# Performance work log

Measured on AMD Instinct MI355X. Metric: run time of the kernel, lower is better.

The kernel has to match this reference:

```python
import jax, jax.numpy as jnp
import numpy as np

LN_EPS = 1e-5

def setup_inputs() -> dict:
    key = jax.random.key(0)
    k1, k2, k3, k4 = jax.random.split(key, 4)
    B, S, D, P = 8, 4096, 1024, 512
    return {
        "hidden_states": jax.random.normal(k1, (B, S, D), dtype=jnp.float32),
        "ln_weight": jnp.ones((D,), dtype=jnp.float32),
        "ln_bias": jnp.zeros((D,), dtype=jnp.float32),
        "W": jax.random.normal(k2, (D, P), dtype=jnp.float32) * 0.02,  # torch Linear weight [out, in]
        "b": jnp.zeros((D,), dtype=jnp.float32),
        "s3_index": jax.random.randint(k3, (P,), 0, D, dtype=jnp.int32),
        "s5_index": jax.random.randint(k4, (D,), 0, D, dtype=jnp.int32),
    }

def reference(hidden_states, ln_weight, ln_bias, W, b, s3_index, s5_index):
    # LayerNorm over last dim
    mu = jnp.mean(hidden_states, axis=-1, keepdims=True)
    var = jnp.mean(jnp.square(hidden_states - mu), axis=-1, keepdims=True)
    normed = (hidden_states - mu) * jax.lax.rsqrt(var + LN_EPS) * ln_weight + ln_bias
    # gather pruned channels, small GEMM 512 -> 1024
    gathered = normed[..., s3_index]                      # [B, S, 512]
    h = jnp.einsum('bsp,dp->bsd', gathered, W) + b        # [B, S, 1024]
    # scatter-add into residual (duplicate indices accumulate, like index_add)
    out = hidden_states.at[..., s5_index].add(h)
    return out
```

## Files before the change

kernel.cpp:

```cpp
#include <hip/hip_runtime.h>
#include <hip/hip_bf16.h>
#include <stdint.h>

#define LN_EPS 1e-5f

typedef __attribute__((ext_vector_type(4))) float f32x4;
typedef __attribute__((ext_vector_type(8))) short bf16x8;

#define D_ 1024
#define P_ 512
#define N_ 32768

__device__ __forceinline__ void gload_lds16(const void* gsrc, void* ldst) {
  __builtin_amdgcn_global_load_lds(
      (const __attribute__((address_space(1))) void*)gsrc,
      (__attribute__((address_space(3))) void*)ldst,
      16, 0, 0);
}

__global__ void k_scatter(const float* __restrict__ W, const float* __restrict__ bias,
                          const int* __restrict__ s5,
                          float* __restrict__ w2f, float* __restrict__ b2) {
  int d = blockIdx.x;
  int c = s5[d];
  const float* wrow = W + (size_t)d * P_;
  float* dst = w2f + (size_t)c * P_;
  for (int p = threadIdx.x; p < P_; p += 256)
    atomicAdd(&dst[p], wrow[p]);
  if (threadIdx.x == 0) atomicAdd(&b2[c], bias[d]);
}

__global__ void k_conv(const float* __restrict__ w2f, __hip_bfloat16* __restrict__ w2b) {
  int i = blockIdx.x * 256 + threadIdx.x;
  if (i < D_ * P_) w2b[i] = __float2bfloat16(w2f[i]);
}

__global__ __launch_bounds__(256) void k_ln_gather(
    const float* __restrict__ x, const float* __restrict__ lnw,
    const float* __restrict__ lnb, const int* __restrict__ s3,
    __hip_bfloat16* __restrict__ g) {
  __shared__ float row[D_];
  __shared__ float psum[4], psum2[4];
  const int n = blockIdx.x;
  const int t = threadIdx.x;
  const float* xr = x + (size_t)n * D_;
  float4 v = ((const float4*)xr)[t];
  ((float4*)row)[t] = v;
  float s  = v.x + v.y + v.z + v.w;
  float s2 = v.x*v.x + v.y*v.y + v.z*v.z + v.w*v.w;
  #pragma unroll
  for (int off = 32; off > 0; off >>= 1) {
    s  += __shfl_down(s, off);
    s2 += __shfl_down(s2, off);
  }
  const int lane = t & 63, wid = t >> 6;
  if (lane == 0) { psum[wid] = s; psum2[wid] = s2; }
  __syncthreads();
  const float tot  = psum[0] + psum[1] + psum[2] + psum[3];
  const float tot2 = psum2[0] + psum2[1] + psum2[2] + psum2[3];
  const float mu  = tot * (1.f / D_);
  const float var = tot2 * (1.f / D_) - mu * mu;
  const float inv = rsqrtf(var + LN_EPS);
  __hip_bfloat16* gr = g + (size_t)n * P_;
  const int i0 = s3[2*t], i1 = s3[2*t+1];
  const float v0 = (row[i0] - mu) * inv * lnw[i0] + lnb[i0];
  const float v1 = (row[i1] - mu) * inv * lnw[i1] + lnb[i1];
  union { __hip_bfloat16 h; unsigned short u; } c0, c1;
  c0.h = __float2bfloat16(v0);
  c1.h = __float2bfloat16(v1);
  unsigned int packed = (unsigned int)c0.u | ((unsigned int)c1.u << 16);
  ((unsigned int*)gr)[t] = packed;
}

#define BM 128
#define BN 128
#define BK 64

__global__ __launch_bounds__(512, 4) void k_gemm(
    const __hip_bfloat16* __restrict__ g,
    const __hip_bfloat16* __restrict__ w2b,
    const float* __restrict__ b2,
    const float* __restrict__ hid,
    float* __restrict__ out) {
  __shared__ __align__(16) char smem[65536];
  char* At[2] = { smem,         smem + 16384 };
  char* Bt[2] = { smem + 32768, smem + 49152 };
  float* ctile = (float*)smem;

  const int bid = blockIdx.x;
  const int x = bid & 7;
  const int kq = bid >> 3;
  const int bm = (x * 32 + (kq >> 3)) * BM;
  const int bn = (kq & 7) * BN;

  const int t = threadIdx.x;
  const int lane = t & 63;
  const int wid = t >> 6;
  const int wr = wid >> 2, wc = wid & 3;

  f32x4 acc[4][2] = {};

  #define STAGE(ks, buf)                                                      \
    {                                                                         \
      const int k0 = (ks) * BK;                                               \
      _Pragma("unroll")                                                       \
      for (int i = 0; i < 2; ++i) {                                           \
        int ch = t + i * 512;                                     \
        int r  = ch >> 3;                      \
        int cc = ch & 7;                                                      \
        int col = ((cc ^ (r & 7)) << 3);       \
        gload_lds16(g   + (size_t)(bm + r) * P_ + k0 + col, At[buf] + ch * 16); \
        gload_lds16(w2b + (size_t)(bn + r) * P_ + k0 + col, Bt[buf] + ch * 16); \
      }                                                                       \
    }

  STAGE(0, 0);
  for (int ks = 0; ks < 8; ++ks) {
    const int buf = ks & 1;
    __syncthreads();
    if (ks < 7) STAGE(ks + 1, buf ^ 1);

    bf16x8 af[2][4], bfr[2][2];
    #pragma unroll
    for (int kk = 0; kk < 2; ++kk) {
      const int colb = kk * 64 + ((lane >> 4) << 4);
      #pragma unroll
      for (int mi = 0; mi < 4; ++mi) {
        const int r = wr * 64 + mi * 16 + (lane & 15);
        af[kk][mi] = *(const bf16x8*)(At[buf] + ((r * 128 + colb) ^ ((r & 7) << 4)));
      }
      #pragma unroll
      for (int ni = 0; ni < 2; ++ni) {
        const int r = wc * 32 + ni * 16 + (lane & 15);
        bfr[kk][ni] = *(const bf16x8*)(Bt[buf] + ((r * 128 + colb) ^ ((r & 7) << 4)));
      }
    }
    #pragma unroll
    for (int kk = 0; kk < 2; ++kk)
      #pragma unroll
      for (int mi = 0; mi < 4; ++mi)
        #pragma unroll
        for (int ni = 0; ni < 2; ++ni)
          acc[mi][ni] = __builtin_amdgcn_mfma_f32_16x16x32_bf16(
              af[kk][mi], bfr[kk][ni], acc[kk ? mi : mi][ni], 0, 0, 0);
  }

  __syncthreads();
  #pragma unroll
  for (int ni = 0; ni < 2; ++ni) {
    #pragma unroll
    for (int mi = 0; mi < 4; ++mi) {
      #pragma unroll
      for (int r4 = 0; r4 < 4; ++r4) {
        const int row = wr * 64 + mi * 16 + ((lane >> 4) << 2) + r4;
        const int col = wc * 32 + ni * 16 + (lane & 15);
        ctile[row * 128 + (col ^ (((row >> 2) & 1) << 4))] = acc[mi][ni][r4];
      }
    }
  }
  __syncthreads();
  #pragma unroll
  for (int i = 0; i < 8; ++i) {
    const int idx = i * 512 + t;
    const int row = idx >> 5;
    const int j0  = (idx & 31) << 2;
    const int swz = ((row >> 2) & 1) << 4;
    const f32x4 a = *(const f32x4*)&ctile[row * 128 + (j0 ^ swz)];
    const f32x4 bias = *(const f32x4*)(b2 + bn + j0);
    const size_t gidx = (size_t)(bm + row) * D_ + bn + j0;
    const f32x4 h = __builtin_nontemporal_load((const f32x4*)(hid + gidx));
    f32x4 o;
    o.x = h.x + a.x + bias.x;
    o.y = h.y + a.y + bias.y;
    o.z = h.z + a.z + bias.z;
    o.w = h.w + a.w + bias.w;
    __builtin_nontemporal_store(o, (f32x4*)(out + gidx));
  }
}

extern "C" void kernel_launch(void* const* d_in, const int* in_sizes, int n_in,
                              void* d_out, int out_size, void* d_ws, size_t ws_size,
                              hipStream_t stream) {
  const float* hid  = (const float*)d_in[0];
  const float* lnw  = (const float*)d_in[1];
  const float* lnb  = (const float*)d_in[2];
  const float* W    = (const float*)d_in[3];
  const float* bias = (const float*)d_in[4];
  const int*   s3   = (const int*)d_in[5];
  const int*   s5   = (const int*)d_in[6];
  float* out = (float*)d_out;

  char* ws = (char*)d_ws;
  float*          w2f = (float*)ws;
  float*          b2  = (float*)(ws + 2097152);
  __hip_bfloat16* w2b = (__hip_bfloat16*)(ws + 2101248);
  __hip_bfloat16* g   = (__hip_bfloat16*)(ws + 3149824);

  hipMemsetAsync(ws, 0, 2101248, stream);
  k_scatter<<<dim3(1024), dim3(256), 0, stream>>>(W, bias, s5, w2f, b2);
  k_conv   <<<dim3(2048), dim3(256), 0, stream>>>(w2f, w2b);
  k_ln_gather<<<dim3(N_), dim3(256), 0, stream>>>(hid, lnw, lnb, s3, g);
  k_gemm   <<<dim3(2048), dim3(512), 0, stream>>>(g, w2b, b2, hid, out);
}
```

Baseline: 122.0 us.

## Replace atomic weight scatter with gather kernel and batch LayerNorm rows per wave

Removes the memset, the atomic scatter kernel and the fp32-to-bf16 conversion kernel. They are replaced by one kernel in which each output channel scans s5 in shared memory and sums the matching W rows directly into bf16. The LayerNorm kernel now processes four rows per wave with no block-level sync, loads the gathered ln weight and bias once per thread, and writes 16-byte bf16 vectors. The goal is fewer launches, no atomics, and less per-row overhead in LN, at the cost of a 1024-iteration serial scan per channel in the weight kernel.

```diff
diff --git a/kernel.cpp b/kernel.cpp
--- a/kernel.cpp
+++ b/kernel.cpp
@@ -18,58 +18,83 @@
       16, 0, 0);
 }
 
-__global__ void k_scatter(const float* __restrict__ W, const float* __restrict__ bias,
-                          const int* __restrict__ s5,
-                          float* __restrict__ w2f, float* __restrict__ b2) {
-  int d = blockIdx.x;
-  int c = s5[d];
-  const float* wrow = W + (size_t)d * P_;
-  float* dst = w2f + (size_t)c * P_;
-  for (int p = threadIdx.x; p < P_; p += 256)
-    atomicAdd(&dst[p], wrow[p]);
-  if (threadIdx.x == 0) atomicAdd(&b2[c], bias[d]);
-}
-
-__global__ void k_conv(const float* __restrict__ w2f, __hip_bfloat16* __restrict__ w2b) {
-  int i = blockIdx.x * 256 + threadIdx.x;
-  if (i < D_ * P_) w2b[i] = __float2bfloat16(w2f[i]);
-}
-
-__global__ __launch_bounds__(256) void k_ln_gather(
+__device__ __forceinline__ short f2bf(float x) {
+  union { __hip_bfloat16 h; short s; } u; u.h = __float2bfloat16(x); return u.s;
+}
+
+__global__ __launch_bounds__(256) void k_w2(
+    const float* __restrict__ W, const float* __restrict__ bias,
+    const int* __restrict__ s5,
+    __hip_bfloat16* __restrict__ w2b, float* __restrict__ b2) {
+  __shared__ int s5l[1024];
+  const int c = blockIdx.x;
+  const int t = threadIdx.x;
+  #pragma unroll
+  for (int i = 0; i < 4; ++i) s5l[t + i * 256] = s5[t + i * 256];
+  __syncthreads();
+  float a0 = 0.f, a1 = 0.f, bb = 0.f;
+  for (int d = 0; d < 1024; ++d) {
+    if (s5l[d] == c) {
+      const float2 wv = ((const float2*)(W + (size_t)d * P_))[t];
+      a0 += wv.x; a1 += wv.y; bb += bias[d];
+    }
+  }
+  const unsigned lo = (unsigned short)f2bf(a0);
+  const unsigned hi = (unsigned short)f2bf(a1);
+  ((unsigned int*)w2b)[c * 256 + t] = lo | (hi << 16);
+  if (t == 0) b2[c] = bb;
+}
+
+__global__ __launch_bounds__(256) void k_ln(
     const float* __restrict__ x, const float* __restrict__ lnw,
     const float* __restrict__ lnb, const int* __restrict__ s3,
     __hip_bfloat16* __restrict__ g) {
-  __shared__ float row[D_];
-  __shared__ float psum[4], psum2[4];
-  const int n = blockIdx.x;
+  __shared__ __align__(16) float rowbuf[4][D_];
   const int t = threadIdx.x;
-  const float* xr = x + (size_t)n * D_;
-  float4 v = ((const float4*)xr)[t];
-  ((float4*)row)[t] = v;
-  float s  = v.x + v.y + v.z + v.w;
-  float s2 = v.x*v.x + v.y*v.y + v.z*v.z + v.w*v.w;
-  #pragma unroll
-  for (int off = 32; off > 0; off >>= 1) {
-    s  += __shfl_down(s, off);
-    s2 += __shfl_down(s2, off);
-  }
   const int lane = t & 63, wid = t >> 6;
-  if (lane == 0) { psum[wid] = s; psum2[wid] = s2; }
-  __syncthreads();
-  const float tot  = psum[0] + psum[1] + psum[2] + psum[3];
-  const float tot2 = psum2[0] + psum2[1] + psum2[2] + psum2[3];
-  const float mu  = tot * (1.f / D_);
-  const float var = tot2 * (1.f / D_) - mu * mu;
-  const float inv = rsqrtf(var + LN_EPS);
-  __hip_bfloat16* gr = g + (size_t)n * P_;
-  const int i0 = s3[2*t], i1 = s3[2*t+1];
-  const float v0 = (row[i0] - mu) * inv * lnw[i0] + lnb[i0];
-  const float v1 = (row[i1] - mu) * inv * lnw[i1] + lnb[i1];
-  union { __hip_bfloat16 h; unsigned short u; } c0, c1;
-  c0.h = __float2bfloat16(v0);
-  c1.h = __float2bfloat16(v1);
-  unsigned int packed = (unsigned int)c0.u | ((unsigned int)c1.u << 16);
-  ((unsigned int*)gr)[t] = packed;
+  float* rb = rowbuf[wid];
+
+  const int4 i0 = ((const int4*)s3)[lane * 2];
+  const int4 i1 = ((const int4*)s3)[lane * 2 + 1];
+  float wv[8], av[8];
+  wv[0]=lnw[i0.x]; wv[1]=lnw[i0.y]; wv[2]=lnw[i0.z]; wv[3]=lnw[i0.w];
+  wv[4]=lnw[i1.x]; wv[5]=lnw[i1.y]; wv[6]=lnw[i1.z]; wv[7]=lnw[i1.w];
+  av[0]=lnb[i0.x]; av[1]=lnb[i0.y]; av[2]=lnb[i0.z]; av[3]=lnb[i0.w];
+  av[4]=lnb[i1.x]; av[5]=lnb[i1.y]; av[6]=lnb[i1.z]; av[7]=lnb[i1.w];
+
+  const int nbase = blockIdx.x * 16 + wid * 4;
+  for (int rr = 0; rr < 4; ++rr) {
+    const int n = nbase + rr;
+    const float* xr = x + (size_t)n * D_;
+    f32x4 v[4];
+    #pragma unroll
+    for (int j = 0; j < 4; ++j) v[j] = ((const f32x4*)xr)[j * 64 + lane];
+    float s = 0.f, s2 = 0.f;
+    #pragma unroll
+    for (int j = 0; j < 4; ++j) {
+      s  += v[j].x + v[j].y + v[j].z + v[j].w;
+      s2 += v[j].x*v[j].x + v[j].y*v[j].y + v[j].z*v[j].z + v[j].w*v[j].w;
+    }
+    #pragma unroll
+    for (int j = 0; j < 4; ++j) ((f32x4*)rb)[j * 64 + lane] = v[j];
+    #pragma unroll
+    for (int off = 32; off > 0; off >>= 1) {
+      s  += __shfl_xor(s, off);
+      s2 += __shfl_xor(s2, off);
+    }
+    const float mu  = s * (1.f / D_);
+    const float inv = rsqrtf(s2 * (1.f / D_) - mu * mu + LN_EPS);
+    bf16x8 gv;
+    gv[0] = f2bf((rb[i0.x] - mu) * inv * wv[0] + av[0]);
+    gv[1] = f2bf((rb[i0.y] - mu) * inv * wv[1] + av[1]);
+    gv[2] = f2bf((rb[i0.z] - mu) * inv * wv[2] + av[2]);
+    gv[3] = f2bf((rb[i0.w] - mu) * inv * wv[3] + av[3]);
+    gv[4] = f2bf((rb[i1.x] - mu) * inv * wv[4] + av[4]);
+    gv[5] = f2bf((rb[i1.y] - mu) * inv * wv[5] + av[5]);
+    gv[6] = f2bf((rb[i1.z] - mu) * inv * wv[6] + av[6]);
+    gv[7] = f2bf((rb[i1.w] - mu) * inv * wv[7] + av[7]);
+    *(bf16x8*)(g + (size_t)n * P_ + lane * 8) = gv;
+  }
 }
 
 #define BM 128
@@ -142,7 +167,7 @@
         #pragma unroll
         for (int ni = 0; ni < 2; ++ni)
           acc[mi][ni] = __builtin_amdgcn_mfma_f32_16x16x32_bf16(
-              af[kk][mi], bfr[kk][ni], acc[kk ? mi : mi][ni], 0, 0, 0);
+              af[kk][mi], bfr[kk][ni], acc[mi][ni], 0, 0, 0);
   }
 
   __syncthreads();
@@ -191,14 +216,11 @@
   float* out = (float*)d_out;
 
   char* ws = (char*)d_ws;
-  float*          w2f = (float*)ws;
-  float*          b2  = (float*)(ws + 2097152);
-  __hip_bfloat16* w2b = (__hip_bfloat16*)(ws + 2101248);
-  __hip_bfloat16* g   = (__hip_bfloat16*)(ws + 3149824);
-
-  hipMemsetAsync(ws, 0, 2101248, stream);
-  k_scatter<<<dim3(1024), dim3(256), 0, stream>>>(W, bias, s5, w2f, b2);
-  k_conv   <<<dim3(2048), dim3(256), 0, stream>>>(w2f, w2b);
-  k_ln_gather<<<dim3(N_), dim3(256), 0, stream>>>(hid, lnw, lnb, s3, g);
-  k_gemm   <<<dim3(2048), dim3(512), 0, stream>>>(g, w2b, b2, hid, out);
-}
+  __hip_bfloat16* w2b = (__hip_bfloat16*)ws;
+  float*          b2  = (float*)(ws + 1048576);
+  __hip_bfloat16* g   = (__hip_bfloat16*)(ws + 1052672);
+
+  k_w2  <<<dim3(1024),  dim3(256), 0, stream>>>(W, bias, s5, w2b, b2);
+  k_ln  <<<dim3(2048),  dim3(256), 0, stream>>>(hid, lnw, lnb, s3, g);
+  k_gemm<<<dim3(2048),  dim3(512), 0, stream>>>(g, w2b, b2, hid, out);
+}
```

Measured after the change: 147.3 us. 1.21x slower.

## Fuse weight scatter, bf16 conversion and LayerNorm gather into one pre-kernel

Applied to the files above, without the earlier changes.

Replaces the memset, atomic scatter of W rows, and separate bf16 conversion kernel with a gather-style formulation. Each output channel block scans s5 to collect its source rows and sums them without global atomics. The pass is merged with the LayerNorm+gather kernel into a single launch, leaving two launches instead of five. Each weight block must scan the full index array, and the per-block loop length depends on index duplication.

```diff
diff --git a/kernel.cpp b/kernel.cpp
--- a/kernel.cpp
+++ b/kernel.cpp
@@ -18,58 +18,79 @@
       16, 0, 0);
 }
 
-__global__ void k_scatter(const float* __restrict__ W, const float* __restrict__ bias,
-                          const int* __restrict__ s5,
-                          float* __restrict__ w2f, float* __restrict__ b2) {
-  int d = blockIdx.x;
-  int c = s5[d];
-  const float* wrow = W + (size_t)d * P_;
-  float* dst = w2f + (size_t)c * P_;
-  for (int p = threadIdx.x; p < P_; p += 256)
-    atomicAdd(&dst[p], wrow[p]);
-  if (threadIdx.x == 0) atomicAdd(&b2[c], bias[d]);
-}
-
-__global__ void k_conv(const float* __restrict__ w2f, __hip_bfloat16* __restrict__ w2b) {
-  int i = blockIdx.x * 256 + threadIdx.x;
-  if (i < D_ * P_) w2b[i] = __float2bfloat16(w2f[i]);
-}
-
-__global__ __launch_bounds__(256) void k_ln_gather(
-    const float* __restrict__ x, const float* __restrict__ lnw,
-    const float* __restrict__ lnb, const int* __restrict__ s3,
-    __hip_bfloat16* __restrict__ g) {
-  __shared__ float row[D_];
+__device__ __forceinline__ short f2bf(float x) {
+  union { __hip_bfloat16 h; short s; } u; u.h = __float2bfloat16(x); return u.s;
+}
+
+__global__ __launch_bounds__(256) void k_pre(
+    const float* __restrict__ x,
+    const float* __restrict__ lnw, const float* __restrict__ lnb,
+    const int* __restrict__ s3,
+    const float* __restrict__ W,
+    const float* __restrict__ bias,
+    const int* __restrict__ s5,
+    __hip_bfloat16* __restrict__ g,
+    __hip_bfloat16* __restrict__ w2b,
+    float* __restrict__ b2) {
+  __shared__ int ibuf[1024];
   __shared__ float psum[4], psum2[4];
-  const int n = blockIdx.x;
+  __shared__ int list[32];
+  __shared__ int cnt;
+  const int bid = blockIdx.x;
   const int t = threadIdx.x;
-  const float* xr = x + (size_t)n * D_;
-  float4 v = ((const float4*)xr)[t];
-  ((float4*)row)[t] = v;
-  float s  = v.x + v.y + v.z + v.w;
-  float s2 = v.x*v.x + v.y*v.y + v.z*v.z + v.w*v.w;
-  #pragma unroll
-  for (int off = 32; off > 0; off >>= 1) {
-    s  += __shfl_down(s, off);
-    s2 += __shfl_down(s2, off);
-  }
-  const int lane = t & 63, wid = t >> 6;
-  if (lane == 0) { psum[wid] = s; psum2[wid] = s2; }
-  __syncthreads();
-  const float tot  = psum[0] + psum[1] + psum[2] + psum[3];
-  const float tot2 = psum2[0] + psum2[1] + psum2[2] + psum2[3];
-  const float mu  = tot * (1.f / D_);
-  const float var = tot2 * (1.f / D_) - mu * mu;
-  const float inv = rsqrtf(var + LN_EPS);
-  __hip_bfloat16* gr = g + (size_t)n * P_;
-  const int i0 = s3[2*t], i1 = s3[2*t+1];
-  const float v0 = (row[i0] - mu) * inv * lnw[i0] + lnb[i0];
-  const float v1 = (row[i1] - mu) * inv * lnw[i1] + lnb[i1];
-  union { __hip_bfloat16 h; unsigned short u; } c0, c1;
-  c0.h = __float2bfloat16(v0);
-  c1.h = __float2bfloat16(v1);
-  unsigned int packed = (unsigned int)c0.u | ((unsigned int)c1.u << 16);
-  ((unsigned int*)gr)[t] = packed;
+
+  if (bid < 1024) {
+    const int c = bid;
+    if (t == 0) cnt = 0;
+    #pragma unroll
+    for (int i = 0; i < 4; ++i) ibuf[t + i * 256] = s5[t + i * 256];
+    __syncthreads();
+    #pragma unroll
+    for (int i = 0; i < 4; ++i) {
+      const int d = t + i * 256;
+      if (ibuf[d] == c) { const int p = atomicAdd(&cnt, 1); list[p] = d; }
+    }
+    __syncthreads();
+    const int k = cnt;
+    float a0 = 0.f, a1 = 0.f, bb = 0.f;
+    for (int j = 0; j < k; ++j) {
+      const int d = list[j];
+      const float2 wv = ((const float2*)(W + (size_t)d * P_))[t];
+      a0 += wv.x; a1 += wv.y; bb += bias[d];
+    }
+    const unsigned lo = (unsigned short)f2bf(a0);
+    const unsigned hi = (unsigned short)f2bf(a1);
+    ((unsigned int*)w2b)[c * 256 + t] = lo | (hi << 16);
+    if (t == 0) b2[c] = bb;
+  } else {
+    const int n = bid - 1024;
+    float* row = (float*)ibuf;
+    const float* xr = x + (size_t)n * D_;
+    float4 v = ((const float4*)xr)[t];
+    ((float4*)row)[t] = v;
+    float s  = v.x + v.y + v.z + v.w;
+    float s2 = v.x*v.x + v.y*v.y + v.z*v.z + v.w*v.w;
+    #pragma unroll
+    for (int off = 32; off > 0; off >>= 1) {
+      s  += __shfl_down(s, off);
+      s2 += __shfl_down(s2, off);
+    }
+    const int lane = t & 63, wid = t >> 6;
+    if (lane == 0) { psum[wid] = s; psum2[wid] = s2; }
+    __syncthreads();
+    const float tot  = psum[0] + psum[1] + psum[2] + psum[3];
+    const float tot2 = psum2[0] + psum2[1] + psum2[2] + psum2[3];
+    const float mu  = tot * (1.f / D_);
+    const float var = tot2 * (1.f / D_) - mu * mu;
+    const float inv = rsqrtf(var + LN_EPS);
+    __hip_bfloat16* gr = g + (size_t)n * P_;
+    const int i0 = s3[2*t], i1 = s3[2*t+1];
+    const float v0 = (row[i0] - mu) * inv * lnw[i0] + lnb[i0];
+    const float v1 = (row[i1] - mu) * inv * lnw[i1] + lnb[i1];
+    const unsigned lo = (unsigned short)f2bf(v0);
+    const unsigned hi = (unsigned short)f2bf(v1);
+    ((unsigned int*)gr)[t] = lo | (hi << 16);
+  }
 }
 
 #define BM 128
@@ -142,7 +163,7 @@
         #pragma unroll
         for (int ni = 0; ni < 2; ++ni)
           acc[mi][ni] = __builtin_amdgcn_mfma_f32_16x16x32_bf16(
-              af[kk][mi], bfr[kk][ni], acc[kk ? mi : mi][ni], 0, 0, 0);
+              af[kk][mi], bfr[kk][ni], acc[mi][ni], 0, 0, 0);
   }
 
   __syncthreads();
@@ -191,14 +212,11 @@
   float* out = (float*)d_out;
 
   char* ws = (char*)d_ws;
-  float*          w2f = (float*)ws;
-  float*          b2  = (float*)(ws + 2097152);
-  __hip_bfloat16* w2b = (__hip_bfloat16*)(ws + 2101248);
-  __hip_bfloat16* g   = (__hip_bfloat16*)(ws + 3149824);
-
-  hipMemsetAsync(ws, 0, 2101248, stream);
-  k_scatter<<<dim3(1024), dim3(256), 0, stream>>>(W, bias, s5, w2f, b2);
-  k_conv   <<<dim3(2048), dim3(256), 0, stream>>>(w2f, w2b);
-  k_ln_gather<<<dim3(N_), dim3(256), 0, stream>>>(hid, lnw, lnb, s3, g);
-  k_gemm   <<<dim3(2048), dim3(512), 0, stream>>>(g, w2b, b2, hid, out);
-}
+  __hip_bfloat16* w2b = (__hip_bfloat16*)ws;
+  float*          b2  = (float*)(ws + 1048576);
+  __hip_bfloat16* g   = (__hip_bfloat16*)(ws + 1052672);
+
+  k_pre <<<dim3(1024 + N_), dim3(256), 0, stream>>>(hid, lnw, lnb, s3, W, bias, s5,
+                                                    g, w2b, b2);
+  k_gemm<<<dim3(2048),      dim3(512), 0, stream>>>(g, w2b, b2, hid, out);
+}
```

Result: faster. 110.7 us (-9.3%).
